# Performance work log

Measured on AMD Instinct MI355X. Metric: run time of the kernel, lower is better.

The kernel has to match this reference:

```python
import jax, jax.numpy as jnp
import numpy as np

D_MODEL = 128
VOCAB = 4096
N_LAYERS = 4
D_FF = 512
D_INNER = 2 * D_MODEL      # Mamba expand=2
D_STATE = 16               # Mamba default
D_CONV = 4                 # Mamba default
DT_RANK = 8                # ceil(d_model/16)
B, L = 8, 4096


def setup_inputs() -> dict:
    key = jax.random.key(0)
    ks = jax.random.split(key, 12)
    def n(k, shp, sc=0.02):
        return jax.random.normal(k, shp, dtype=jnp.float32) * sc
    A0 = jnp.tile(jnp.arange(1, D_STATE + 1, dtype=jnp.float32)[None, None, :], (N_LAYERS, D_INNER, 1))
    return {
        "tokens": jax.random.randint(ks[0], (B, L), 0, VOCAB),
        "emb": n(ks[1], (VOCAB, D_MODEL)),
        "ln_w": jnp.ones((N_LAYERS, D_MODEL), jnp.float32),
        "ln_b": jnp.zeros((N_LAYERS, D_MODEL), jnp.float32),
        "W_in": n(ks[2], (N_LAYERS, D_MODEL, 2 * D_INNER)),
        "conv_w": n(ks[3], (N_LAYERS, D_INNER, 1, D_CONV), 0.2),
        "conv_b": jnp.zeros((N_LAYERS, D_INNER), jnp.float32),
        "W_xproj": n(ks[4], (N_LAYERS, D_INNER, DT_RANK + 2 * D_STATE)),
        "W_dt": n(ks[5], (N_LAYERS, DT_RANK, D_INNER), 0.1),
        "b_dt": jnp.full((N_LAYERS, D_INNER), -4.6, jnp.float32),  # softplus ~ 0.01
        "A_log": jnp.log(A0),
        "D_skip": jnp.ones((N_LAYERS, D_INNER), jnp.float32),
        "W_out": n(ks[6], (N_LAYERS, D_INNER, D_MODEL)),
        "W1": n(ks[7], (D_MODEL, D_FF)),
        "b1": jnp.zeros((D_FF,), jnp.float32),
        "W2": n(ks[8], (D_FF, VOCAB)),
        "b2": jnp.zeros((VOCAB,), jnp.float32),
    }


def _layer_norm(x, w, b):
    mu = x.mean(-1, keepdims=True)
    var = ((x - mu) ** 2).mean(-1, keepdims=True)
    return (x - mu) * jax.lax.rsqrt(var + 1e-5) * w + b


def _mamba(x, W_in, conv_w, conv_b, W_xproj, W_dt, b_dt, A_log, D_skip, W_out):
    # x: [B, L, d_model]
    xz = jnp.einsum('bld,de->ble', x, W_in)          # [B, L, 2*d_inner]
    xc, z = jnp.split(xz, 2, axis=-1)
    # depthwise causal conv over time
    xt = xc.swapaxes(1, 2)                            # [B, d_inner, L]
    xt = jax.lax.conv_general_dilated(
        xt, conv_w, window_strides=(1,), padding=[(D_CONV - 1, 0)],
        feature_group_count=D_INNER,
        dimension_numbers=('NCH', 'OIH', 'NCH')) + conv_b[None, :, None]
    u = jax.nn.silu(xt).swapaxes(1, 2)                # [B, L, d_inner]
    dbc = jnp.einsum('bld,de->ble', u, W_xproj)
    dt_r = dbc[..., :DT_RANK]
    Bm = dbc[..., DT_RANK:DT_RANK + D_STATE]          # [B, L, d_state]
    Cm = dbc[..., DT_RANK + D_STATE:]                 # [B, L, d_state]
    dt = jax.nn.softplus(jnp.einsum('blr,rd->bld', dt_r, W_dt) + b_dt)
    A = -jnp.exp(A_log)                               # [d_inner, d_state]

    def step(h, t):
        dt_t, B_t, C_t, u_t = t                       # [B,di], [B,ds], [B,ds], [B,di]
        dA = jnp.exp(dt_t[..., None] * A)             # [B, di, ds]
        h = dA * h + (dt_t * u_t)[..., None] * B_t[:, None, :]
        y = jnp.einsum('bds,bs->bd', h, C_t)
        return h, y

    xs = (dt.swapaxes(0, 1), Bm.swapaxes(0, 1), Cm.swapaxes(0, 1), u.swapaxes(0, 1))
    h0 = jnp.zeros((x.shape[0], D_INNER, D_STATE), x.dtype)
    _, ys = jax.lax.scan(step, h0, xs)                # [L, B, d_inner]
    y = ys.swapaxes(0, 1) + u * D_skip
    y = y * jax.nn.silu(z)
    return jnp.einsum('bld,de->ble', y, W_out)


def reference(tokens, emb, ln_w, ln_b, W_in, conv_w, conv_b, W_xproj, W_dt,
              b_dt, A_log, D_skip, W_out, W1, b1, W2, b2):
    x = emb[tokens]                                   # [B, L, d_model]
    for i in range(N_LAYERS):
        # source discards the residual returned by Block: x = mixer(norm(x))
        x = _mamba(_layer_norm(x, ln_w[i], ln_b[i]), W_in[i], conv_w[i],
                   conv_b[i], W_xproj[i], W_dt[i], b_dt[i], A_log[i],
                   D_skip[i], W_out[i])
    h = jax.nn.relu(jnp.einsum('bld,df->blf', x, W1) + b1)
    return jnp.einsum('blf,fv->blv', h, W2) + b2
```

## Files before the change

### kernel.cpp

```cpp
#include <hip/hip_runtime.h>
#include <hip/hip_bf16.h>

typedef __hip_bfloat16 bf16;
typedef __attribute__((ext_vector_type(8))) short short8;
typedef __attribute__((ext_vector_type(4))) float floatx4;
typedef __attribute__((ext_vector_type(16))) float floatx16;

#define D_MODEL 128
#define VOCAB   4096
#define N_LAYERS 4
#define D_FF    512
#define D_INNER 256
#define D_STATE 16
#define DT_RANK 8
#define BATCH   8
#define SEQ     4096
#define NTOK    (BATCH*SEQ)
#define NCHUNK  16
#define CHUNK   256

__device__ __forceinline__ float bf2f(bf16 v) { return __bfloat162float(v); }
__device__ __forceinline__ bf16  f2bf(float v) { return __float2bfloat16(v); }

__device__ __forceinline__ void load_lds16(const void* g, void* l) {
  __builtin_amdgcn_global_load_lds(
      (const __attribute__((address_space(1))) unsigned int*)g,
      (__attribute__((address_space(3))) unsigned int*)l, 16, 0, 0);
}

__device__ __forceinline__ void store_out(float* p, float v) { *p = v; }
__device__ __forceinline__ void store_out(bf16* p, float v) { *p = f2bf(v); }

#define WT_TOTAL 2686976
__global__ void convw_kernel(const float* __restrict__ W_in,
                             const float* __restrict__ W_xproj,
                             const float* __restrict__ W_out,
                             const float* __restrict__ W1,
                             const float* __restrict__ W2,
                             bf16* __restrict__ Wt) {
  for (int o = blockIdx.x * blockDim.x + threadIdx.x; o < WT_TOTAL;
       o += gridDim.x * blockDim.x) {
    float v;
    if (o < 262144) {
      int l = o >> 16, r = o & 65535, n = r >> 7, k = r & 127;
      v = W_in[l * 65536 + k * 512 + n];
    } else if (o < 393216) {
      int p = o - 262144, l = p >> 15, r = p & 32767, n = r >> 8, k = r & 255;
      v = (n < 40) ? W_xproj[l * 10240 + k * 40 + n] : 0.f;
    } else if (o < 524288) {
      int p = o - 393216, l = p >> 15, r = p & 32767, n = r >> 8, k = r & 255;
      v = W_out[l * 32768 + k * 128 + n];
    } else if (o < 589824) {
      int p = o - 524288, n = p >> 7, k = p & 127;
      v = W1[k * 512 + n];
    } else {
      int p = o - 589824, n = p >> 9, k = p & 511;
      v = W2[k * 4096 + n];
    }
    Wt[o] = f2bf(v);
  }
}

__global__ void embed_kernel(const int* __restrict__ tokens,
                             const float* __restrict__ emb,
                             float* __restrict__ X) {
  int idx = blockIdx.x * 256 + threadIdx.x;
  int bl = idx >> 5, c = idx & 31;
  int tok = tokens[bl];
  ((float4*)X)[(long)bl * 32 + c] = ((const float4*)emb)[(long)tok * 32 + c];
}

__global__ __launch_bounds__(256) void ln_kernel(const float* __restrict__ X,
                                                 const float* __restrict__ w,
                                                 const float* __restrict__ b,
                                                 bf16* __restrict__ XN) {
  int wv = threadIdx.x >> 6, lane = threadIdx.x & 63;
  long row = (long)blockIdx.x * 4 + wv;
  const float* xp = X + row * 128;
  float2 v = *(const float2*)(xp + lane * 2);
  float s = v.x + v.y, q = v.x * v.x + v.y * v.y;
  #pragma unroll
  for (int o = 32; o; o >>= 1) {
    s += __shfl_xor(s, o, 64);
    q += __shfl_xor(q, o, 64);
  }
  float mu = s * (1.f / 128.f);
  float var = q * (1.f / 128.f) - mu * mu;
  float rs = rsqrtf(var + 1e-5f);
  int c = lane * 2;
  float o0 = (v.x - mu) * rs * w[c] + b[c];
  float o1 = (v.y - mu) * rs * w[c + 1] + b[c + 1];
  bf16* op = XN + row * 128 + c;
  op[0] = f2bf(o0);
  op[1] = f2bf(o1);
}

template <typename OutT>
__global__ __launch_bounds__(256) void gemm_kernel(
    const bf16* __restrict__ A, const bf16* __restrict__ Bt,
    OutT* __restrict__ C, const float* __restrict__ bias,
    int K, int N, int relu) {
  __shared__ __align__(16) bf16 As[128 * 64];
  __shared__ __align__(16) bf16 Bs[128 * 64];
  const int tid = threadIdx.x;
  const int lane = tid & 63;
  const int wave = tid >> 6;
  const int m0 = blockIdx.x * 128;
  const int n0 = blockIdx.y * 128;
  const int wm = (wave >> 1) * 64;
  const int wn = (wave & 1) * 64;
  floatx4 acc[4][4] = {};

  const int lrow = lane >> 3;
  const int lcol = (lane & 7) * 8;
  for (int k0 = 0; k0 < K; k0 += 64) {
    #pragma unroll
    for (int j = 0; j < 4; ++j) {
      int qq = wave * 4 + j;
      int row = qq * 8 + lrow;
      load_lds16(A + (long)(m0 + row) * K + k0 + lcol, &As[(qq * 8) * 64]);
      load_lds16(Bt + (long)(n0 + row) * K + k0 + lcol, &Bs[(qq * 8) * 64]);
    }
    __syncthreads();
    #pragma unroll
    for (int kk = 0; kk < 64; kk += 32) {
      short8 af[4], bfr[4];
      const int fr = lane & 15;
      const int fq = (lane >> 4) * 8 + kk;
      #pragma unroll
      for (int i = 0; i < 4; ++i) {
        af[i]  = *(const short8*)&As[(wm + i * 16 + fr) * 64 + fq];
        bfr[i] = *(const short8*)&Bs[(wn + i * 16 + fr) * 64 + fq];
      }
      #pragma unroll
      for (int mi = 0; mi < 4; ++mi)
        #pragma unroll
        for (int ni = 0; ni < 4; ++ni)
          acc[mi][ni] = __builtin_amdgcn_mfma_f32_16x16x32_bf16(
              af[mi], bfr[ni], acc[mi][ni], 0, 0, 0);
    }
    __syncthreads();
  }
  const int cr = (lane >> 4) * 4;
  const int cc = lane & 15;
  #pragma unroll
  for (int ni = 0; ni < 4; ++ni) {
    int col = n0 + wn + ni * 16 + cc;
    if (col >= N) continue;
    float bv = bias ? bias[col] : 0.f;
    #pragma unroll
    for (int mi = 0; mi < 4; ++mi) {
      #pragma unroll
      for (int r = 0; r < 4; ++r) {
        int row = m0 + wm + mi * 16 + cr + r;
        float v = acc[mi][ni][r] + bv;
        if (relu) v = fmaxf(v, 0.f);
        store_out(&C[(long)row * N + col], v);
      }
    }
  }
}

template <typename OutT>
__global__ __launch_bounds__(512, 2) void gemm256_kernel(
    const bf16* __restrict__ A, const bf16* __restrict__ Bt,
    OutT* __restrict__ C, const float* __restrict__ bias,
    int K, int N, int ntiles, int relu) {
  __shared__ __align__(16) bf16 sA[2][256 * 32];
  __shared__ __align__(16) bf16 sB[2][256 * 32];
  const int tid  = threadIdx.x;
  const int lane = tid & 63;
  const int wave = tid >> 6;
  const int wm = (wave >> 2) << 7;
  const int wn = (wave & 3) << 6;

  const int nwg = gridDim.x;
  const int cpx = nwg >> 3;
  const int id  = ((int)blockIdx.x & 7) * cpx + ((int)blockIdx.x >> 3);
  const int bm = id / ntiles, bn = id - bm * ntiles;
  const long m0 = (long)bm << 8;
  const long n0 = (long)bn << 8;

  const bf16* Ab = A + m0 * K;
  const bf16* Bb = Bt + n0 * K;

  const int srow = lane >> 2;
  const int sgl  = (((lane & 3) ^ (srow & 3)) << 3);
  const int NT = K >> 5;

  const int wh16  = (wave & 3) << 4;
  const int aoff0 = (wave < 4) ? wh16 : (128 + wh16);
  const int aoff1 = aoff0 + 64;

#define STAGE(src, dst, r0, k0)                                           \
  load_lds16((src) + (long)((r0) + srow) * K + (k0) + sgl, (dst) + (r0) * 32)

  STAGE(Ab, sA[0], aoff0, 0);
  STAGE(Bb, sB[0], aoff0, 0);
  STAGE(Bb, sB[0], aoff1, 0);
  STAGE(Ab, sA[0], aoff1, 0);

  floatx16 acc[4][2] = {};
  const int frow = lane & 31;
  const int fg   = lane >> 5;

  for (int t = 0; t < NT; ++t) {
    const int cur = t & 1, nxt = cur ^ 1;
    const int kn = (t + 1 < NT) ? ((t + 1) << 5) : 0;
    const bf16* cA = sA[cur];
    const bf16* cB = sB[cur];

    asm volatile("s_waitcnt vmcnt(1)" ::: "memory");
    asm volatile("s_barrier" ::: "memory");
    STAGE(Ab, sA[nxt], aoff0, kn);
    STAGE(Bb, sB[nxt], aoff0, kn);
    short8 a0[2][2], b0[2][2];
    #pragma unroll
    for (int mi = 0; mi < 2; ++mi)
      #pragma unroll
      for (int kk = 0; kk < 2; ++kk) {
        int r = wm + mi * 32 + frow;
        int g = kk * 2 + fg;
        a0[mi][kk] = *(const short8*)&cA[r * 32 + ((g ^ (r & 3)) << 3)];
      }
    #pragma unroll
    for (int ni = 0; ni < 2; ++ni)
      #pragma unroll
      for (int kk = 0; kk < 2; ++kk) {
        int r = wn + ni * 32 + frow;
        int g = kk * 2 + fg;
        b0[ni][kk] = *(const short8*)&cB[r * 32 + ((g ^ (r & 3)) << 3)];
      }
    __builtin_amdgcn_s_setprio(1);
    #pragma unroll
    for (int mi = 0; mi < 2; ++mi)
      #pragma unroll
      for (int ni = 0; ni < 2; ++ni)
        #pragma unroll
        for (int kk = 0; kk < 2; ++kk)
          acc[mi][ni] = __builtin_amdgcn_mfma_f32_32x32x16_bf16(
              a0[mi][kk], b0[ni][kk], acc[mi][ni], 0, 0, 0);
    __builtin_amdgcn_s_setprio(0);

    asm volatile("s_waitcnt vmcnt(2)" ::: "memory");
    asm volatile("s_barrier" ::: "memory");
    STAGE(Bb, sB[nxt], aoff1, kn);
    STAGE(Ab, sA[nxt], aoff1, kn);
    short8 a1[2][2];
    #pragma unroll
    for (int mi = 0; mi < 2; ++mi)
      #pragma unroll
      for (int kk = 0; kk < 2; ++kk) {
        int r = wm + 64 + mi * 32 + frow;
        int g = kk * 2 + fg;
        a1[mi][kk] = *(const short8*)&cA[r * 32 + ((g ^ (r & 3)) << 3)];
      }
    __builtin_amdgcn_s_setprio(1);
    #pragma unroll
    for (int mi = 0; mi < 2; ++mi)
      #pragma unroll
      for (int ni = 0; ni < 2; ++ni)
        #pragma unroll
        for (int kk = 0; kk < 2; ++kk)
          acc[2 + mi][ni] = __builtin_amdgcn_mfma_f32_32x32x16_bf16(
              a1[mi][kk], b0[ni][kk], acc[2 + mi][ni], 0, 0, 0);
    __builtin_amdgcn_s_setprio(0);
  }
#undef STAGE

  #pragma unroll
  for (int mi = 0; mi < 4; ++mi)
    #pragma unroll
    for (int ni = 0; ni < 2; ++ni) {
      long col = n0 + wn + ni * 32 + frow;
      float bv = bias ? bias[col] : 0.f;
      #pragma unroll
      for (int r = 0; r < 16; ++r) {
        long row = m0 + wm + mi * 32 + (r & 3) + ((r >> 2) << 3) + (fg << 2);
        float v = acc[mi][ni][r] + bv;
        if (relu) v = fmaxf(v, 0.f);
        store_out(&C[row * N + col], v);
      }
    }
}

__global__ __launch_bounds__(256) void conv_silu_kernel(
    const float* __restrict__ XZ, const float* __restrict__ conv_w,
    const float* __restrict__ conv_b, bf16* __restrict__ U,
    bf16* __restrict__ G) {
  int d = threadIdx.x;
  long bl = blockIdx.x;
  int t = (int)(bl & (SEQ - 1));
  float w0 = conv_w[d * 4 + 0], w1 = conv_w[d * 4 + 1];
  float w2 = conv_w[d * 4 + 2], w3 = conv_w[d * 4 + 3];
  const float* xp = XZ + bl * 512 + d;
  float acc = conv_b[d] + w3 * xp[0];
  if (t >= 1) acc += w2 * xp[-512];
  if (t >= 2) acc += w1 * xp[-1024];
  if (t >= 3) acc += w0 * xp[-1536];
  float su = acc / (1.f + __expf(-acc));
  float z = xp[256];
  float g = z / (1.f + __expf(-z));
  U[bl * 256 + d] = f2bf(su);
  G[bl * 256 + d] = f2bf(g);
}

__global__ __launch_bounds__(256) void dtprep_kernel(
    const float* __restrict__ DBC, const float* __restrict__ W_dt,
    const float* __restrict__ b_dt, float* __restrict__ DTo) {
  __shared__ float r8[8];
  int d = threadIdx.x;
  long bl = blockIdx.x;
  if (d < 8) r8[d] = DBC[bl * 40 + d];
  __syncthreads();
  float acc = b_dt[d];
  #pragma unroll
  for (int r = 0; r < 8; ++r) acc = fmaf(r8[r], W_dt[r * 256 + d], acc);
  float dt = (acc > 15.f) ? acc : log1pf(__expf(acc));
  DTo[bl * 256 + d] = dt;
}

__global__ __launch_bounds__(256) void scan_pass1_kernel(
    const float* __restrict__ DT, const bf16* __restrict__ U,
    const float* __restrict__ DBC, const float* __restrict__ A_log,
    float* __restrict__ CSP, float* __restrict__ CSS) {
  int s = threadIdx.x & 15, dd = threadIdx.x >> 4;
  int d = blockIdx.x * 16 + dd;
  int c = blockIdx.y, b = blockIdx.z;
  float A2 = -__expf(A_log[d * 16 + s]) * 1.44269504088896f;
  long t0 = (long)b * SEQ + (long)c * CHUNK;
  const float* dtp = DT + t0 * 256 + d;
  const bf16* up = U + t0 * 256 + d;
  const float* bp = DBC + t0 * 40 + 8 + s;
  float h = 0.f, P = 1.f;
  #pragma unroll 4
  for (int t = 0; t < CHUNK; ++t) {
    float dt = *dtp;
    float u = bf2f(*up);
    float Bv = *bp;
    float a = __builtin_amdgcn_exp2f(dt * A2);
    h = fmaf(a, h, dt * u * Bv);
    P *= a;
    dtp += 256; up += 256; bp += 40;
  }
  int idx = (b * 16 + c) * 4096 + d * 16 + s;
  CSP[idx] = P;
  CSS[idx] = h;
}

__global__ __launch_bounds__(256) void scan_combine_kernel(
    const float* __restrict__ P, const float* __restrict__ S,
    float* __restrict__ HI) {
  int id = blockIdx.x * 256 + threadIdx.x;
  int b = id >> 12, ds = id & 4095;
  float h = 0.f;
  #pragma unroll
  for (int c = 0; c < NCHUNK; ++c) {
    int idx = ((b * 16 + c) << 12) + ds;
    HI[idx] = h;
    h = S[idx] + P[idx] * h;
  }
}

__global__ __launch_bounds__(256) void scan_pass2_kernel(
    const float* __restrict__ DT, const bf16* __restrict__ U,
    const float* __restrict__ DBC, const bf16* __restrict__ G,
    const float* __restrict__ HI, const float* __restrict__ A_log,
    const float* __restrict__ D_skip, bf16* __restrict__ Y) {
  int s = threadIdx.x & 15, dd = threadIdx.x >> 4;
  int d = blockIdx.x * 16 + dd;
  int c = blockIdx.y, b = blockIdx.z;
  float A2 = -__expf(A_log[d * 16 + s]) * 1.44269504088896f;
  float Dv = D_skip[d];
  long t0 = (long)b * SEQ + (long)c * CHUNK;
  const float* dtp = DT + t0 * 256 + d;
  const bf16* up = U + t0 * 256 + d;
  const bf16* gp = G + t0 * 256 + d;
  const float* bp = DBC + t0 * 40 + 8 + s;
  bf16* yp = Y + t0 * 256 + d;
  int idx = (b * 16 + c) * 4096 + d * 16 + s;
  float h = HI[idx];
  #pragma unroll 4
  for (int t = 0; t < CHUNK; ++t) {
    float dt = *dtp;
    float u = bf2f(*up);
    float Bv = *bp;
    float Cv = bp[16];
    float a = __builtin_amdgcn_exp2f(dt * A2);
    h = fmaf(a, h, dt * u * Bv);
    float p = h * Cv;
    p += __shfl_xor(p, 8, 16);
    p += __shfl_xor(p, 4, 16);
    p += __shfl_xor(p, 2, 16);
    p += __shfl_xor(p, 1, 16);
    if (s == 0) {
      float g = bf2f(*gp);
      *yp = f2bf((p + u * Dv) * g);
    }
    dtp += 256; up += 256; gp += 256; bp += 40; yp += 256;
  }
}

extern "C" void kernel_launch(void* const* d_in, const int* in_sizes, int n_in,
                              void* d_out, int out_size, void* d_ws,
                              size_t ws_size, hipStream_t stream) {
  const int*   tokens  = (const int*)d_in[0];
  const float* emb     = (const float*)d_in[1];
  const float* ln_w    = (const float*)d_in[2];
  const float* ln_b    = (const float*)d_in[3];
  const float* W_in    = (const float*)d_in[4];
  const float* conv_w  = (const float*)d_in[5];
  const float* conv_b  = (const float*)d_in[6];
  const float* W_xproj = (const float*)d_in[7];
  const float* W_dt    = (const float*)d_in[8];
  const float* b_dt    = (const float*)d_in[9];
  const float* A_log   = (const float*)d_in[10];
  const float* D_skip  = (const float*)d_in[11];
  const float* W_out   = (const float*)d_in[12];
  const float* W1      = (const float*)d_in[13];
  const float* b1      = (const float*)d_in[14];
  const float* W2      = (const float*)d_in[15];
  const float* b2      = (const float*)d_in[16];

  char* ws = (char*)d_ws;
  float* X    = (float*)(ws + 0);
  float* XZ   = (float*)(ws + 16777216);
  bf16*  XN   = (bf16*) (ws + 83886080);
  bf16*  U    = (bf16*) (ws + 92274688);
  bf16*  G    = (bf16*) (ws + 109051904);
  float* DBC  = (float*)(ws + 125829120);
  float* DT   = (float*)(ws + 131072000);
  bf16*  Y    = (bf16*) (ws + 164626432);
  float* CSP  = (float*)(ws + 181403648);
  float* CSS  = (float*)(ws + 183500800);
  float* HI   = (float*)(ws + 185597952);
  bf16*  Wt   = (bf16*) (ws + 187695104);
  bf16*  H    = (bf16*) XZ;
  bf16*  XBF  = XN;

  bf16* Wt_in  = Wt;
  bf16* Wt_xp  = Wt + 262144;
  bf16* Wt_out = Wt + 393216;
  bf16* Wt_1   = Wt + 524288;
  bf16* Wt_2   = Wt + 589824;

  convw_kernel<<<2048, 256, 0, stream>>>(W_in, W_xproj, W_out, W1, W2, Wt);
  embed_kernel<<<4096, 256, 0, stream>>>(tokens, emb, X);

  for (int i = 0; i < N_LAYERS; ++i) {
    ln_kernel<<<8192, 256, 0, stream>>>(X, ln_w + i * 128, ln_b + i * 128, XN);
    gemm256_kernel<float><<<256, 512, 0, stream>>>(
        XN, Wt_in + i * 65536, XZ, nullptr, 128, 512, 2, 0);
    conv_silu_kernel<<<32768, 256, 0, stream>>>(
        XZ, conv_w + i * 1024, conv_b + i * 256, U, G);
    gemm_kernel<float><<<dim3(256, 1), 256, 0, stream>>>(
        U, Wt_xp + i * 32768, DBC, nullptr, 256, 40, 0);
    dtprep_kernel<<<32768, 256, 0, stream>>>(
        DBC, W_dt + i * 2048, b_dt + i * 256, DT);
    scan_pass1_kernel<<<dim3(16, 16, 8), 256, 0, stream>>>(
        DT, U, DBC, A_log + i * 4096, CSP, CSS);
    scan_combine_kernel<<<128, 256, 0, stream>>>(CSP, CSS, HI);
    scan_pass2_kernel<<<dim3(16, 16, 8), 256, 0, stream>>>(
        DT, U, DBC, G, HI, A_log + i * 4096, D_skip + i * 256, Y);
    if (i < N_LAYERS - 1) {
      gemm_kernel<float><<<dim3(256, 1), 256, 0, stream>>>(
          Y, Wt_out + i * 32768, X, nullptr, 256, 128, 0);
    } else {
      gemm_kernel<bf16><<<dim3(256, 1), 256, 0, stream>>>(
          Y, Wt_out + i * 32768, XBF, nullptr, 256, 128, 0);
    }
  }

  gemm256_kernel<bf16><<<256, 512, 0, stream>>>(
      XBF, Wt_1, H, b1, 128, 512, 2, 1);
  gemm256_kernel<float><<<2048, 512, 0, stream>>>(
      H, Wt_2, (float*)d_out, b2, 512, 4096, 16, 0);
}
```

Measured before the change: 2.213 ms.

## Fuse layernorm into embed and out-proj GEMM, store XZ/DT in bf16, swizzle LDS

```diff
diff --git a/kernel.cpp b/kernel.cpp
--- a/kernel.cpp
+++ b/kernel.cpp
@@ -61,22 +61,14 @@
   }
 }
 
-__global__ void embed_kernel(const int* __restrict__ tokens,
-                             const float* __restrict__ emb,
-                             float* __restrict__ X) {
-  int idx = blockIdx.x * 256 + threadIdx.x;
-  int bl = idx >> 5, c = idx & 31;
-  int tok = tokens[bl];
-  ((float4*)X)[(long)bl * 32 + c] = ((const float4*)emb)[(long)tok * 32 + c];
-}
-
-__global__ __launch_bounds__(256) void ln_kernel(const float* __restrict__ X,
-                                                 const float* __restrict__ w,
-                                                 const float* __restrict__ b,
-                                                 bf16* __restrict__ XN) {
+__global__ __launch_bounds__(256) void embln_kernel(
+    const int* __restrict__ tokens, const float* __restrict__ emb,
+    const float* __restrict__ w, const float* __restrict__ b,
+    bf16* __restrict__ XN) {
   int wv = threadIdx.x >> 6, lane = threadIdx.x & 63;
   long row = (long)blockIdx.x * 4 + wv;
-  const float* xp = X + row * 128;
+  int tok = tokens[row];
+  const float* xp = emb + (long)tok * 128;
   float2 v = *(const float2*)(xp + lane * 2);
   float s = v.x + v.y, q = v.x * v.x + v.y * v.y;
   #pragma unroll
@@ -95,11 +87,11 @@
   op[1] = f2bf(o1);
 }
 
-template <typename OutT>
+template <typename OutT, int EPI>
 __global__ __launch_bounds__(256) void gemm_kernel(
     const bf16* __restrict__ A, const bf16* __restrict__ Bt,
-    OutT* __restrict__ C, const float* __restrict__ bias,
-    int K, int N, int relu) {
+    OutT* __restrict__ C, const float* __restrict__ lnw,
+    const float* __restrict__ lnb, int K, int N) {
   __shared__ __align__(16) bf16 As[128 * 64];
   __shared__ __align__(16) bf16 Bs[128 * 64];
   const int tid = threadIdx.x;
@@ -112,7 +104,7 @@
   floatx4 acc[4][4] = {};
 
   const int lrow = lane >> 3;
-  const int lcol = (lane & 7) * 8;
+  const int lcol = ((lane & 7) ^ lrow) * 8;
   for (int k0 = 0; k0 < K; k0 += 64) {
     #pragma unroll
     for (int j = 0; j < 4; ++j) {
@@ -126,11 +118,13 @@
     for (int kk = 0; kk < 64; kk += 32) {
       short8 af[4], bfr[4];
       const int fr = lane & 15;
-      const int fq = (lane >> 4) * 8 + kk;
+      const int q  = (lane >> 4) + (kk >> 3);
       #pragma unroll
       for (int i = 0; i < 4; ++i) {
-        af[i]  = *(const short8*)&As[(wm + i * 16 + fr) * 64 + fq];
-        bfr[i] = *(const short8*)&Bs[(wn + i * 16 + fr) * 64 + fq];
+        int ra = wm + i * 16 + fr;
+        int rb = wn + i * 16 + fr;
+        af[i]  = *(const short8*)&As[ra * 64 + ((q ^ (ra & 7)) << 3)];
+        bfr[i] = *(const short8*)&Bs[rb * 64 + ((q ^ (rb & 7)) << 3)];
       }
       #pragma unroll
       for (int mi = 0; mi < 4; ++mi)
@@ -143,19 +137,61 @@
   }
   const int cr = (lane >> 4) * 4;
   const int cc = lane & 15;
-  #pragma unroll
-  for (int ni = 0; ni < 4; ++ni) {
-    int col = n0 + wn + ni * 16 + cc;
-    if (col >= N) continue;
-    float bv = bias ? bias[col] : 0.f;
-    #pragma unroll
-    for (int mi = 0; mi < 4; ++mi) {
+
+  if (EPI == 2) {
+    float* lnS = (float*)As;
+    float* lnQ = lnS + 256;
+    #pragma unroll
+    for (int mi = 0; mi < 4; ++mi)
       #pragma unroll
       for (int r = 0; r < 4; ++r) {
-        int row = m0 + wm + mi * 16 + cr + r;
-        float v = acc[mi][ni][r] + bv;
-        if (relu) v = fmaxf(v, 0.f);
-        store_out(&C[(long)row * N + col], v);
+        float s = 0.f, qs = 0.f;
+        #pragma unroll
+        for (int ni = 0; ni < 4; ++ni) {
+          float v = acc[mi][ni][r];
+          s += v; qs += v * v;
+        }
+        #pragma unroll
+        for (int o = 1; o < 16; o <<= 1) {
+          s  += __shfl_xor(s, o, 64);
+          qs += __shfl_xor(qs, o, 64);
+        }
+        if (cc == 0) {
+          int row = wm + mi * 16 + cr + r;
+          lnS[row * 2 + (wave & 1)] = s;
+          lnQ[row * 2 + (wave & 1)] = qs;
+        }
+      }
+    __syncthreads();
+    #pragma unroll
+    for (int mi = 0; mi < 4; ++mi)
+      #pragma unroll
+      for (int r = 0; r < 4; ++r) {
+        int row = wm + mi * 16 + cr + r;
+        float tot  = lnS[row * 2] + lnS[row * 2 + 1];
+        float totq = lnQ[row * 2] + lnQ[row * 2 + 1];
+        float mu = tot * (1.f / 128.f);
+        float var = totq * (1.f / 128.f) - mu * mu;
+        float rs = rsqrtf(var + 1e-5f);
+        #pragma unroll
+        for (int ni = 0; ni < 4; ++ni) {
+          int col = wn + ni * 16 + cc;
+          float v = (acc[mi][ni][r] - mu) * rs * lnw[col] + lnb[col];
+          store_out(&C[(long)(m0 + row) * 128 + col], v);
+        }
+      }
+  } else {
+    #pragma unroll
+    for (int ni = 0; ni < 4; ++ni) {
+      int col = n0 + wn + ni * 16 + cc;
+      if (col >= N) continue;
+      #pragma unroll
+      for (int mi = 0; mi < 4; ++mi) {
+        #pragma unroll
+        for (int r = 0; r < 4; ++r) {
+          int row = m0 + wm + mi * 16 + cr + r;
+          store_out(&C[(long)row * N + col], acc[mi][ni][r]);
+        }
       }
     }
   }
@@ -285,7 +321,7 @@
 }
 
 __global__ __launch_bounds__(256) void conv_silu_kernel(
-    const float* __restrict__ XZ, const float* __restrict__ conv_w,
+    const bf16* __restrict__ XZ, const float* __restrict__ conv_w,
     const float* __restrict__ conv_b, bf16* __restrict__ U,
     bf16* __restrict__ G) {
   int d = threadIdx.x;
@@ -293,13 +329,13 @@
   int t = (int)(bl & (SEQ - 1));
   float w0 = conv_w[d * 4 + 0], w1 = conv_w[d * 4 + 1];
   float w2 = conv_w[d * 4 + 2], w3 = conv_w[d * 4 + 3];
-  const float* xp = XZ + bl * 512 + d;
-  float acc = conv_b[d] + w3 * xp[0];
-  if (t >= 1) acc += w2 * xp[-512];
-  if (t >= 2) acc += w1 * xp[-1024];
-  if (t >= 3) acc += w0 * xp[-1536];
+  const bf16* xp = XZ + bl * 512 + d;
+  float acc = conv_b[d] + w3 * bf2f(xp[0]);
+  if (t >= 1) acc += w2 * bf2f(xp[-512]);
+  if (t >= 2) acc += w1 * bf2f(xp[-1024]);
+  if (t >= 3) acc += w0 * bf2f(xp[-1536]);
   float su = acc / (1.f + __expf(-acc));
-  float z = xp[256];
+  float z = bf2f(xp[256]);
   float g = z / (1.f + __expf(-z));
   U[bl * 256 + d] = f2bf(su);
   G[bl * 256 + d] = f2bf(g);
@@ -307,7 +343,7 @@
 
 __global__ __launch_bounds__(256) void dtprep_kernel(
     const float* __restrict__ DBC, const float* __restrict__ W_dt,
-    const float* __restrict__ b_dt, float* __restrict__ DTo) {
+    const float* __restrict__ b_dt, bf16* __restrict__ DTo) {
   __shared__ float r8[8];
   int d = threadIdx.x;
   long bl = blockIdx.x;
@@ -317,11 +353,11 @@
   #pragma unroll
   for (int r = 0; r < 8; ++r) acc = fmaf(r8[r], W_dt[r * 256 + d], acc);
   float dt = (acc > 15.f) ? acc : log1pf(__expf(acc));
-  DTo[bl * 256 + d] = dt;
+  DTo[bl * 256 + d] = f2bf(dt);
 }
 
 __global__ __launch_bounds__(256) void scan_pass1_kernel(
-    const float* __restrict__ DT, const bf16* __restrict__ U,
+    const bf16* __restrict__ DT, const bf16* __restrict__ U,
     const float* __restrict__ DBC, const float* __restrict__ A_log,
     float* __restrict__ CSP, float* __restrict__ CSS) {
   int s = threadIdx.x & 15, dd = threadIdx.x >> 4;
@@ -329,13 +365,13 @@
   int c = blockIdx.y, b = blockIdx.z;
   float A2 = -__expf(A_log[d * 16 + s]) * 1.44269504088896f;
   long t0 = (long)b * SEQ + (long)c * CHUNK;
-  const float* dtp = DT + t0 * 256 + d;
+  const bf16* dtp = DT + t0 * 256 + d;
   const bf16* up = U + t0 * 256 + d;
   const float* bp = DBC + t0 * 40 + 8 + s;
   float h = 0.f, P = 1.f;
   #pragma unroll 4
   for (int t = 0; t < CHUNK; ++t) {
-    float dt = *dtp;
+    float dt = bf2f(*dtp);
     float u = bf2f(*up);
     float Bv = *bp;
     float a = __builtin_amdgcn_exp2f(dt * A2);
@@ -363,7 +399,7 @@
 }
 
 __global__ __launch_bounds__(256) void scan_pass2_kernel(
-    const float* __restrict__ DT, const bf16* __restrict__ U,
+    const bf16* __restrict__ DT, const bf16* __restrict__ U,
     const float* __restrict__ DBC, const bf16* __restrict__ G,
     const float* __restrict__ HI, const float* __restrict__ A_log,
     const float* __restrict__ D_skip, bf16* __restrict__ Y) {
@@ -373,7 +409,7 @@
   float A2 = -__expf(A_log[d * 16 + s]) * 1.44269504088896f;
   float Dv = D_skip[d];
   long t0 = (long)b * SEQ + (long)c * CHUNK;
-  const float* dtp = DT + t0 * 256 + d;
+  const bf16* dtp = DT + t0 * 256 + d;
   const bf16* up = U + t0 * 256 + d;
   const bf16* gp = G + t0 * 256 + d;
   const float* bp = DBC + t0 * 40 + 8 + s;
@@ -382,7 +418,7 @@
   float h = HI[idx];
   #pragma unroll 4
   for (int t = 0; t < CHUNK; ++t) {
-    float dt = *dtp;
+    float dt = bf2f(*dtp);
     float u = bf2f(*up);
     float Bv = *bp;
     float Cv = bp[16];
@@ -423,13 +459,12 @@
   const float* b2      = (const float*)d_in[16];
 
   char* ws = (char*)d_ws;
-  float* X    = (float*)(ws + 0);
-  float* XZ   = (float*)(ws + 16777216);
+  bf16*  XZ   = (bf16*) (ws + 16777216);
   bf16*  XN   = (bf16*) (ws + 83886080);
   bf16*  U    = (bf16*) (ws + 92274688);
   bf16*  G    = (bf16*) (ws + 109051904);
   float* DBC  = (float*)(ws + 125829120);
-  float* DT   = (float*)(ws + 131072000);
+  bf16*  DT   = (bf16*) (ws + 131072000);
   bf16*  Y    = (bf16*) (ws + 164626432);
   float* CSP  = (float*)(ws + 181403648);
   float* CSS  = (float*)(ws + 183500800);
@@ -445,16 +480,15 @@
   bf16* Wt_2   = Wt + 589824;
 
   convw_kernel<<<2048, 256, 0, stream>>>(W_in, W_xproj, W_out, W1, W2, Wt);
-  embed_kernel<<<4096, 256, 0, stream>>>(tokens, emb, X);
+  embln_kernel<<<8192, 256, 0, stream>>>(tokens, emb, ln_w, ln_b, XN);
 
   for (int i = 0; i < N_LAYERS; ++i) {
-    ln_kernel<<<8192, 256, 0, stream>>>(X, ln_w + i * 128, ln_b + i * 128, XN);
-    gemm256_kernel<float><<<256, 512, 0, stream>>>(
+    gemm256_kernel<bf16><<<256, 512, 0, stream>>>(
         XN, Wt_in + i * 65536, XZ, nullptr, 128, 512, 2, 0);
     conv_silu_kernel<<<32768, 256, 0, stream>>>(
         XZ, conv_w + i * 1024, conv_b + i * 256, U, G);
-    gemm_kernel<float><<<dim3(256, 1), 256, 0, stream>>>(
-        U, Wt_xp + i * 32768, DBC, nullptr, 256, 40, 0);
+    gemm_kernel<float, 0><<<dim3(256, 1), 256, 0, stream>>>(
+        U, Wt_xp + i * 32768, DBC, nullptr, nullptr, 256, 40);
     dtprep_kernel<<<32768, 256, 0, stream>>>(
         DBC, W_dt + i * 2048, b_dt + i * 256, DT);
     scan_pass1_kernel<<<dim3(16, 16, 8), 256, 0, stream>>>(
@@ -463,11 +497,12 @@
     scan_pass2_kernel<<<dim3(16, 16, 8), 256, 0, stream>>>(
         DT, U, DBC, G, HI, A_log + i * 4096, D_skip + i * 256, Y);
     if (i < N_LAYERS - 1) {
-      gemm_kernel<float><<<dim3(256, 1), 256, 0, stream>>>(
-          Y, Wt_out + i * 32768, X, nullptr, 256, 128, 0);
+      gemm_kernel<bf16, 2><<<dim3(256, 1), 256, 0, stream>>>(
+          Y, Wt_out + i * 32768, XN, ln_w + (i + 1) * 128,
+          ln_b + (i + 1) * 128, 256, 128);
     } else {
-      gemm_kernel<bf16><<<dim3(256, 1), 256, 0, stream>>>(
-          Y, Wt_out + i * 32768, XBF, nullptr, 256, 128, 0);
+      gemm_kernel<bf16, 0><<<dim3(256, 1), 256, 0, stream>>>(
+          Y, Wt_out + i * 32768, XBF, nullptr, nullptr, 256, 128);
     }
   }
 
```

Result: no change. 2.192 ms (-0.9%).
